# Kernel tuning notes

Measured on AMD Instinct MI355X. Metric: run time of the kernel, lower is better.

## Reference

```python
import jax, jax.numpy as jnp
import numpy as np

NUM_GRAPHS = 512  # number of segments (graphs) in the batch
NEG_SLOPE = 0.01  # nn.LeakyReLU default


def setup_inputs() -> dict:
    key = jax.random.key(0)
    k1, k2, k3, k4, k5 = jax.random.split(key, 5)
    N, D = 200000, 128
    h_topo = jax.random.normal(k1, (N, D), dtype=jnp.float32)
    h_geom = jax.random.normal(k2, (N, D), dtype=jnp.float32)
    batch = jnp.sort(jax.random.randint(k3, (N,), 0, NUM_GRAPHS, dtype=jnp.int64))
    concat_dim, hidden, out_dim = 6 * D, 2 * D, 128
    W1 = jax.random.normal(k4, (concat_dim, hidden), dtype=jnp.float32) * 0.02
    b1 = jnp.zeros((hidden,), dtype=jnp.float32)
    W2 = jax.random.normal(k5, (hidden, out_dim), dtype=jnp.float32) * 0.02
    b2 = jnp.zeros((out_dim,), dtype=jnp.float32)
    return {"h_topo": h_topo, "h_geom": h_geom, "batch": batch,
            "W1": W1, "b1": b1, "W2": W2, "b2": b2}


def _pool_feats(h, batch):
    # global_max_pool / global_mean_pool keyed by graph id, gathered back per node
    gmax = jax.ops.segment_max(h, batch, num_segments=NUM_GRAPHS)
    gsum = jax.ops.segment_sum(h, batch, num_segments=NUM_GRAPHS)
    cnt = jax.ops.segment_sum(jnp.ones((h.shape[0],), h.dtype), batch,
                              num_segments=NUM_GRAPHS)
    gmean = gsum / jnp.maximum(cnt, 1.0)[:, None]
    return gmax[batch], gmean[batch]  # [N, D] each


def reference(h_topo, h_geom, batch, W1, b1, W2, b2):
    t_max, t_mean = _pool_feats(h_topo, batch)
    g_max, g_mean = _pool_feats(h_geom, batch)
    # [Topo, Geom, TopoMax, TopoMean, GeomMax, GeomMean]
    combined = jnp.concatenate(
        [h_topo, t_max, t_mean, h_geom, g_max, g_mean], axis=-1)  # [N, 6D]
    h = combined @ W1 + b1
    h = jnp.where(h >= 0, h, NEG_SLOPE * h)  # LeakyReLU
    return h @ W2 + b2
```

## Files before the change

### kernel.cpp

```cpp
#include <hip/hip_runtime.h>
#include <math.h>

#define NUM_GRAPHS 512
#define D 128
#define NEG 0.01f
#define BN 128
#define NS 4

typedef __attribute__((ext_vector_type(8))) short  bf16x8;
typedef __attribute__((ext_vector_type(4))) float  f32x4;
typedef __attribute__((ext_vector_type(4))) int    i32x4;

__device__ __forceinline__ unsigned short f2bf(float f) {
    unsigned u = __float_as_uint(f);
    u += 0x7fffu + ((u >> 16) & 1u);
    return (unsigned short)(u >> 16);
}

__device__ __forceinline__ bf16x8 cvt8(float4 a, float4 b) {
    unsigned w0, w1, w2, w3;
    asm("v_cvt_pk_bf16_f32 %0, %1, %2" : "=v"(w0) : "v"(a.x), "v"(a.y));
    asm("v_cvt_pk_bf16_f32 %0, %1, %2" : "=v"(w1) : "v"(a.z), "v"(a.w));
    asm("v_cvt_pk_bf16_f32 %0, %1, %2" : "=v"(w2) : "v"(b.x), "v"(b.y));
    asm("v_cvt_pk_bf16_f32 %0, %1, %2" : "=v"(w3) : "v"(b.z), "v"(b.w));
    i32x4 v; v[0] = (int)w0; v[1] = (int)w1; v[2] = (int)w2; v[3] = (int)w3;
    return __builtin_bit_cast(bf16x8, v);
}

__device__ __forceinline__ int swz128(int row, int k) {
    return (row >> 6) * 16384 + (row & 63) * 256 + (k ^ ((row & 7) << 3));
}

#define LDS_BARRIER()                                                        \
    do {                                                                     \
        asm volatile("s_waitcnt lgkmcnt(0)" ::: "memory");                   \
        __builtin_amdgcn_s_barrier();                                        \
        asm volatile("" ::: "memory");                                       \
    } while (0)

#define FMAX4(a, b)                                                          \
    do {                                                                     \
        (a).x = fmaxf((a).x, (b).x); (a).y = fmaxf((a).y, (b).y);            \
        (a).z = fmaxf((a).z, (b).z); (a).w = fmaxf((a).w, (b).w);            \
    } while (0)
#define FADD4(a, b)                                                          \
    do {                                                                     \
        (a).x += (b).x; (a).y += (b).y; (a).z += (b).z; (a).w += (b).w;      \
    } while (0)

__global__ __launch_bounds__(256) void bounds_kernel(
    const int* __restrict__ batch, int N, int* __restrict__ seg)
{
    const int g = blockIdx.x * 256 + threadIdx.x;
    if (g <= NUM_GRAPHS) {
        int lo = 0, hi = N;
        while (lo < hi) { int m = (lo + hi) >> 1; if (batch[m] < g) lo = m + 1; else hi = m; }
        seg[g] = lo;
    }
}

__global__ __launch_bounds__(256) void pool_kernel(
    const float* __restrict__ h_topo, const float* __restrict__ h_geom,
    const int* __restrict__ seg, int N, float* __restrict__ pp)
{
    const int g = blockIdx.x, t = blockIdx.y, s = blockIdx.z;
    const float* __restrict__ h = t ? h_geom : h_topo;

    const int start = seg[g], end = seg[g + 1];
    const int len = end - start;
    const int r0  = start + (int)(((long long)len * s) / NS);
    const int r1  = start + (int)(((long long)len * (s + 1)) / NS);

    const int c = threadIdx.x & 31;
    const int r = threadIdx.x >> 5;

    float4 mxA = make_float4(-INFINITY, -INFINITY, -INFINITY, -INFINITY);
    float4 mxB = mxA, mxC = mxA, mxD = mxA;
    float4 smA = make_float4(0.f, 0.f, 0.f, 0.f);
    float4 smB = smA, smC = smA, smD = smA;

    int row = r0 + r;
    for (; row + 24 < r1; row += 32) {
        float4 v0 = *(const float4*)(h + (size_t)row * D + c * 4);
        float4 v1 = *(const float4*)(h + (size_t)(row + 8)  * D + c * 4);
        float4 v2 = *(const float4*)(h + (size_t)(row + 16) * D + c * 4);
        float4 v3 = *(const float4*)(h + (size_t)(row + 24) * D + c * 4);
        FMAX4(mxA, v0); FADD4(smA, v0);
        FMAX4(mxB, v1); FADD4(smB, v1);
        FMAX4(mxC, v2); FADD4(smC, v2);
        FMAX4(mxD, v3); FADD4(smD, v3);
    }
    for (; row < r1; row += 8) {
        float4 v = *(const float4*)(h + (size_t)row * D + c * 4);
        FMAX4(mxA, v); FADD4(smA, v);
    }
    FMAX4(mxA, mxB); FMAX4(mxC, mxD); FMAX4(mxA, mxC);
    FADD4(smA, smB); FADD4(smC, smD); FADD4(smA, smC);

    __shared__ float4 smx[256], ssm[256];
    smx[threadIdx.x] = mxA; ssm[threadIdx.x] = smA;
    __syncthreads();
    #pragma unroll
    for (int st = 4; st > 0; st >>= 1) {
        if (r < st) {
            float4 a = smx[threadIdx.x + st * 32];
            float4 b = ssm[threadIdx.x + st * 32];
            float4 m0 = smx[threadIdx.x];
            float4 s0 = ssm[threadIdx.x];
            FMAX4(m0, a); FADD4(s0, b);
            smx[threadIdx.x] = m0; ssm[threadIdx.x] = s0;
        }
        __syncthreads();
    }
    if (r == 0) {
        float* dst = pp + ((size_t)(g * 2 + t) * NS + s) * 256;
        *(float4*)(dst + c * 4)       = smx[threadIdx.x];
        *(float4*)(dst + 128 + c * 4) = ssm[threadIdx.x];
    }
}

__global__ __launch_bounds__(256) void pmat_kernel(
    const float* __restrict__ pp, const int* __restrict__ seg,
    const float* __restrict__ W1, const float* __restrict__ b1,
    float* __restrict__ P)
{
    const int g = blockIdx.x;
    const int j = threadIdx.x;

    const int start = seg[g], end = seg[g + 1];
    const float inv   = 1.0f / fmaxf((float)(end - start), 1.0f);
    const bool  empty = (end <= start);

    __shared__ float pl[512];
    #pragma unroll
    for (int e0 = 0; e0 < 2; ++e0) {
        const int e = j + e0 * 256;
        const int t = e >> 8, i = e & 255;
        const float* q = pp + (size_t)(g * 2 + t) * NS * 256 + i;
        float v;
        if (i < 128)
            v = fmaxf(fmaxf(q[0], q[256]), fmaxf(q[512], q[768]));
        else
            v = (q[0] + q[256] + q[512] + q[768]) * inv;
        pl[e] = empty ? 0.f : v;
    }
    __syncthreads();

    float acc = b1[j];
    #pragma unroll 8
    for (int k = 0; k < 256; ++k)
        acc += pl[k] * W1[(size_t)(128 + k) * 256 + j];
    #pragma unroll 8
    for (int k = 0; k < 256; ++k)
        acc += pl[256 + k] * W1[(size_t)(512 + k) * 256 + j];

    P[(size_t)g * 256 + j] = acc;
}

__global__ __launch_bounds__(256) void wconv_kernel(
    const float* __restrict__ W1, const float* __restrict__ W2,
    unsigned short* __restrict__ W1bT, unsigned short* __restrict__ W2bT)
{
    const int idx = blockIdx.x * 256 + threadIdx.x;
    if (idx < 256 * 256) {
        const int n = idx >> 8, k = idx & 255;
        const int kk = (k < 128) ? k : (k + 256);
        W1bT[idx] = f2bf(W1[(size_t)kk * 256 + n]);
    } else {
        const int j = idx - 256 * 256;
        if (j < 128 * 256) {
            const int n = j >> 8, k = j & 255;
            W2bT[j] = f2bf(W2[(size_t)k * 128 + n]);
        }
    }
}

__global__ __launch_bounds__(512, 4) void mlp_mfma(
    const float* __restrict__ h_topo, const float* __restrict__ h_geom,
    const int* __restrict__ batch, const float* __restrict__ P,
    const unsigned short* __restrict__ W1bT, const unsigned short* __restrict__ W2bT,
    const float* __restrict__ b2, float* __restrict__ out, int N)
{
    __shared__ unsigned short xs[128 * 256];
    __shared__ int gid[128];

    const int tid  = threadIdx.x;
    const int wave = tid >> 6, lane = tid & 63;
    const int base = (gridDim.x - 1 - blockIdx.x) * BN;

    {
        const int row  = tid >> 2, kq = tid & 3;
        const int node = min(base + row, N - 1);
        const float* src = (kq < 2) ? h_topo + (size_t)node * D + kq * 64
                                    : h_geom + (size_t)node * D + (kq - 2) * 64;
        #pragma unroll
        for (int i = 0; i < 8; ++i) {
            float4 a = ((const float4*)src)[2 * i];
            float4 b = ((const float4*)src)[2 * i + 1];
            *(bf16x8*)&xs[swz128(row, kq * 64 + i * 8)] = cvt8(a, b);
        }
    }
    if (tid < 128) gid[tid] = batch[min(base + tid, N - 1)];

    const int g0 = batch[base];
    const int g1 = batch[min(base + 127, N - 1)];
    const bool uni = (g0 == g1);

    const int lhi = lane >> 4;
    const int llo = lane & 15;

    const int wr = wave >> 2, wc = wave & 3;

    const unsigned short* w1p = W1bT + (size_t)(wc * 64 + llo) * 256 + lhi * 8;

    float4 pf4[4];
    if (uni) {
        #pragma unroll
        for (int ct = 0; ct < 4; ++ct)
            pf4[ct] = *(const float4*)(P + (size_t)g0 * 256 + wc * 64 + ct * 16 + lhi * 4);
    }

    bf16x8 aW[2][4];
    #pragma unroll
    for (int ct = 0; ct < 4; ++ct) {
        aW[0][ct] = *(const bf16x8*)(w1p + (size_t)ct * 16 * 256);
        aW[1][ct] = *(const bf16x8*)(w1p + (size_t)ct * 16 * 256 + 32);
    }

    LDS_BARRIER();

    f32x4 acc[4][4];
    #pragma unroll
    for (int rt = 0; rt < 4; ++rt)
        #pragma unroll
        for (int ct = 0; ct < 4; ++ct)
            acc[rt][ct] = uni ? (f32x4){pf4[ct].x, pf4[ct].y, pf4[ct].z, pf4[ct].w}
                              : (f32x4){0.f, 0.f, 0.f, 0.f};

    #pragma unroll
    for (int ks = 0; ks < 8; ++ks) {
        const int kb = ks * 32 + lhi * 8;
        bf16x8 bX[4];
        #pragma unroll
        for (int rt = 0; rt < 4; ++rt)
            bX[rt] = *(const bf16x8*)&xs[swz128(wr * 64 + rt * 16 + llo, kb)];
        __builtin_amdgcn_s_setprio(1);
        #pragma unroll
        for (int rt = 0; rt < 4; ++rt)
            #pragma unroll
            for (int ct = 0; ct < 4; ++ct)
                acc[rt][ct] = __builtin_amdgcn_mfma_f32_16x16x32_bf16(
                    aW[ks & 1][ct], bX[rt], acc[rt][ct], 0, 0, 0);
        __builtin_amdgcn_s_setprio(0);
        if (ks < 6) {
            const int kbn = (ks + 2) * 32;
            #pragma unroll
            for (int ct = 0; ct < 4; ++ct)
                aW[ks & 1][ct] = *(const bf16x8*)(w1p + (size_t)ct * 16 * 256 + kbn);
        }
    }

    const int wr2 = wave >> 2, wc2 = wave & 3;
    const unsigned short* w2pA = W2bT + (size_t)(wc2 * 32 + llo) * 256 + lhi * 8;
    const unsigned short* w2pB = W2bT + (size_t)(wc2 * 32 + 16 + llo) * 256 + lhi * 8;

    bf16x8 aW2[2][2];
    aW2[0][0] = *(const bf16x8*)(w2pA);
    aW2[0][1] = *(const bf16x8*)(w2pB);
    aW2[1][0] = *(const bf16x8*)(w2pA + 32);
    aW2[1][1] = *(const bf16x8*)(w2pB + 32);

    LDS_BARRIER();

    #pragma unroll
    for (int rt = 0; rt < 4; ++rt) {
        const int nrow = wr * 64 + rt * 16 + llo;
        int gg = 0;
        if (!uni) gg = gid[nrow];
        #pragma unroll
        for (int ct = 0; ct < 4; ++ct) {
            const int j0 = wc * 64 + ct * 16 + lhi * 4;
            float4 v = make_float4(acc[rt][ct][0], acc[rt][ct][1],
                                   acc[rt][ct][2], acc[rt][ct][3]);
            if (!uni) {
                float4 pv = *(const float4*)(P + (size_t)gg * 256 + j0);
                v.x += pv.x; v.y += pv.y; v.z += pv.z; v.w += pv.w;
            }
            v.x = fmaxf(v.x, NEG * v.x); v.y = fmaxf(v.y, NEG * v.y);
            v.z = fmaxf(v.z, NEG * v.z); v.w = fmaxf(v.w, NEG * v.w);
            unsigned w0, w1;
            asm("v_cvt_pk_bf16_f32 %0, %1, %2" : "=v"(w0) : "v"(v.x), "v"(v.y));
            asm("v_cvt_pk_bf16_f32 %0, %1, %2" : "=v"(w1) : "v"(v.z), "v"(v.w));
            uint2 hw; hw.x = w0; hw.y = w1;
            *(uint2*)&xs[swz128(nrow, j0)] = hw;
        }
    }

    LDS_BARRIER();

    f32x4 acc2[4][2];
    {
        const float4 bbA = *(const float4*)(b2 + wc2 * 32 + lhi * 4);
        const float4 bbB = *(const float4*)(b2 + wc2 * 32 + 16 + lhi * 4);
        #pragma unroll
        for (int nt = 0; nt < 4; ++nt) {
            acc2[nt][0] = (f32x4){bbA.x, bbA.y, bbA.z, bbA.w};
            acc2[nt][1] = (f32x4){bbB.x, bbB.y, bbB.z, bbB.w};
        }
    }
    #pragma unroll
    for (int ks = 0; ks < 8; ++ks) {
        const int kb = ks * 32 + lhi * 8;
        bf16x8 bH[4];
        #pragma unroll
        for (int nt = 0; nt < 4; ++nt)
            bH[nt] = *(const bf16x8*)&xs[swz128(wr2 * 64 + nt * 16 + llo, kb)];
        __builtin_amdgcn_s_setprio(1);
        #pragma unroll
        for (int nt = 0; nt < 4; ++nt) {
            acc2[nt][0] = __builtin_amdgcn_mfma_f32_16x16x32_bf16(
                aW2[ks & 1][0], bH[nt], acc2[nt][0], 0, 0, 0);
            acc2[nt][1] = __builtin_amdgcn_mfma_f32_16x16x32_bf16(
                aW2[ks & 1][1], bH[nt], acc2[nt][1], 0, 0, 0);
        }
        __builtin_amdgcn_s_setprio(0);
        if (ks < 6) {
            aW2[ks & 1][0] = *(const bf16x8*)(w2pA + (ks + 2) * 32);
            aW2[ks & 1][1] = *(const bf16x8*)(w2pB + (ks + 2) * 32);
        }
    }

    #pragma unroll
    for (int nt = 0; nt < 4; ++nt) {
        const int node = base + wr2 * 64 + nt * 16 + llo;
        if (node < N) {
            float* op = out + (size_t)node * 128 + wc2 * 32 + lhi * 4;
            __builtin_nontemporal_store(acc2[nt][0], (f32x4*)op);
            __builtin_nontemporal_store(acc2[nt][1], (f32x4*)(op + 16));
        }
    }
}

extern "C" void kernel_launch(void* const* d_in, const int* in_sizes, int n_in,
                              void* d_out, int out_size, void* d_ws, size_t ws_size,
                              hipStream_t stream)
{
    const float* h_topo = (const float*)d_in[0];
    const float* h_geom = (const float*)d_in[1];
    const int*   batch  = (const int*)  d_in[2];
    const float* W1     = (const float*)d_in[3];
    const float* b1     = (const float*)d_in[4];
    const float* W2     = (const float*)d_in[5];
    const float* b2     = (const float*)d_in[6];
    float* out = (float*)d_out;

    const int N = in_sizes[0] / D;

    float*          pp   = (float*)d_ws;
    float*          P    = pp + (size_t)NUM_GRAPHS * 2 * NS * 256;
    unsigned short* W1bT = (unsigned short*)(P + (size_t)NUM_GRAPHS * 256);
    unsigned short* W2bT = W1bT + 256 * 256;
    int*            seg  = (int*)(W2bT + 128 * 256);

    bounds_kernel<<<3, 256, 0, stream>>>(batch, N, seg);
    wconv_kernel<<<(256 * 256 + 128 * 256) / 256, 256, 0, stream>>>(W1, W2, W1bT, W2bT);
    pool_kernel<<<dim3(NUM_GRAPHS, 2, NS), 256, 0, stream>>>(h_topo, h_geom, seg, N, pp);
    pmat_kernel<<<NUM_GRAPHS, 256, 0, stream>>>(pp, seg, W1, b1, P);

    const int nblocks = (N + BN - 1) / BN;
    mlp_mfma<<<nblocks, 512, 0, stream>>>(h_topo, h_geom, batch, P,
                                          W1bT, W2bT, b2, out, N);
}
```

Before: 194.0 us.

## Halve MLP row tile, swap MFMA operand roles, and split pooling eightfold

The fused MLP kernel now processes 64 nodes per 256-thread block instead of 128 nodes per 512-thread block. Each wave owns a 64-column slice of the hidden layer across all 64 rows, and the MFMA operand order is swapped so node rows come from LDS as the A operand. The hidden-activation epilogue now adds the per-graph term, applies LeakyReLU and writes bf16 to LDS one element at a time instead of packed pairs. The pooling split factor rises from 4 to 8, and the reduce kernel loops over the partials. The aim is more blocks in flight with less LDS per block, at the cost of loading the weight tiles twice as often per node and narrower LDS stores.

```diff
diff --git a/kernel.cpp b/kernel.cpp
--- a/kernel.cpp
+++ b/kernel.cpp
@@ -4,8 +4,8 @@
 #define NUM_GRAPHS 512
 #define D 128
 #define NEG 0.01f
-#define BN 128
-#define NS 4
+#define BN 64
+#define NS 8
 
 typedef __attribute__((ext_vector_type(8))) short  bf16x8;
 typedef __attribute__((ext_vector_type(4))) float  f32x4;
@@ -27,8 +27,8 @@
     return __builtin_bit_cast(bf16x8, v);
 }
 
-__device__ __forceinline__ int swz128(int row, int k) {
-    return (row >> 6) * 16384 + (row & 63) * 256 + (k ^ ((row & 7) << 3));
+__device__ __forceinline__ int swz64(int row, int k) {
+    return row * 256 + (k ^ ((row & 7) << 3));
 }
 
 #define LDS_BARRIER()                                                        \
@@ -138,10 +138,16 @@
         const int t = e >> 8, i = e & 255;
         const float* q = pp + (size_t)(g * 2 + t) * NS * 256 + i;
         float v;
-        if (i < 128)
-            v = fmaxf(fmaxf(q[0], q[256]), fmaxf(q[512], q[768]));
-        else
-            v = (q[0] + q[256] + q[512] + q[768]) * inv;
+        if (i < 128) {
+            v = q[0];
+            #pragma unroll
+            for (int s = 1; s < NS; ++s) v = fmaxf(v, q[s * 256]);
+        } else {
+            v = q[0];
+            #pragma unroll
+            for (int s = 1; s < NS; ++s) v += q[s * 256];
+            v *= inv;
+        }
         pl[e] = empty ? 0.f : v;
     }
     __syncthreads();
@@ -175,14 +181,14 @@
     }
 }
 
-__global__ __launch_bounds__(512, 4) void mlp_mfma(
+__global__ __launch_bounds__(256, 4) void mlp_mfma(
     const float* __restrict__ h_topo, const float* __restrict__ h_geom,
     const int* __restrict__ batch, const float* __restrict__ P,
     const unsigned short* __restrict__ W1bT, const unsigned short* __restrict__ W2bT,
     const float* __restrict__ b2, float* __restrict__ out, int N)
 {
-    __shared__ unsigned short xs[128 * 256];
-    __shared__ int gid[128];
+    __shared__ unsigned short xs[64 * 256];
+    __shared__ int gid[64];
 
     const int tid  = threadIdx.x;
     const int wave = tid >> 6, lane = tid & 63;
@@ -197,34 +203,32 @@
         for (int i = 0; i < 8; ++i) {
             float4 a = ((const float4*)src)[2 * i];
             float4 b = ((const float4*)src)[2 * i + 1];
-            *(bf16x8*)&xs[swz128(row, kq * 64 + i * 8)] = cvt8(a, b);
-        }
-    }
-    if (tid < 128) gid[tid] = batch[min(base + tid, N - 1)];
+            *(bf16x8*)&xs[swz64(row, kq * 64 + i * 8)] = cvt8(a, b);
+        }
+    }
+    if (tid < 64) gid[tid] = batch[min(base + tid, N - 1)];
 
     const int g0 = batch[base];
-    const int g1 = batch[min(base + 127, N - 1)];
+    const int g1 = batch[min(base + 63, N - 1)];
     const bool uni = (g0 == g1);
 
     const int lhi = lane >> 4;
     const int llo = lane & 15;
 
-    const int wr = wave >> 2, wc = wave & 3;
-
-    const unsigned short* w1p = W1bT + (size_t)(wc * 64 + llo) * 256 + lhi * 8;
-
-    float4 pf4[4];
+    const unsigned short* w1p = W1bT + (size_t)(wave * 64 + llo) * 256 + lhi * 8;
+
+    float pf[4];
     if (uni) {
         #pragma unroll
         for (int ct = 0; ct < 4; ++ct)
-            pf4[ct] = *(const float4*)(P + (size_t)g0 * 256 + wc * 64 + ct * 16 + lhi * 4);
-    }
-
-    bf16x8 aW[2][4];
+            pf[ct] = P[(size_t)g0 * 256 + wave * 64 + ct * 16 + llo];
+    }
+
+    bf16x8 bfr[2][4];
     #pragma unroll
     for (int ct = 0; ct < 4; ++ct) {
-        aW[0][ct] = *(const bf16x8*)(w1p + (size_t)ct * 16 * 256);
-        aW[1][ct] = *(const bf16x8*)(w1p + (size_t)ct * 16 * 256 + 32);
+        bfr[0][ct] = *(const bf16x8*)(w1p + (size_t)ct * 16 * 256);
+        bfr[1][ct] = *(const bf16x8*)(w1p + (size_t)ct * 16 * 256 + 32);
     }
 
     LDS_BARRIER();
@@ -233,36 +237,36 @@
     #pragma unroll
     for (int rt = 0; rt < 4; ++rt)
         #pragma unroll
-        for (int ct = 0; ct < 4; ++ct)
-            acc[rt][ct] = uni ? (f32x4){pf4[ct].x, pf4[ct].y, pf4[ct].z, pf4[ct].w}
-                              : (f32x4){0.f, 0.f, 0.f, 0.f};
+        for (int ct = 0; ct < 4; ++ct) {
+            const float p = uni ? pf[ct] : 0.f;
+            acc[rt][ct] = (f32x4){p, p, p, p};
+        }
 
     #pragma unroll
     for (int ks = 0; ks < 8; ++ks) {
         const int kb = ks * 32 + lhi * 8;
-        bf16x8 bX[4];
+        bf16x8 afr[4];
         #pragma unroll
         for (int rt = 0; rt < 4; ++rt)
-            bX[rt] = *(const bf16x8*)&xs[swz128(wr * 64 + rt * 16 + llo, kb)];
+            afr[rt] = *(const bf16x8*)&xs[swz64(rt * 16 + llo, kb)];
         __builtin_amdgcn_s_setprio(1);
         #pragma unroll
         for (int rt = 0; rt < 4; ++rt)
             #pragma unroll
             for (int ct = 0; ct < 4; ++ct)
                 acc[rt][ct] = __builtin_amdgcn_mfma_f32_16x16x32_bf16(
-                    aW[ks & 1][ct], bX[rt], acc[rt][ct], 0, 0, 0);
+                    afr[rt], bfr[ks & 1][ct], acc[rt][ct], 0, 0, 0);
         __builtin_amdgcn_s_setprio(0);
         if (ks < 6) {
             const int kbn = (ks + 2) * 32;
             #pragma unroll
             for (int ct = 0; ct < 4; ++ct)
-                aW[ks & 1][ct] = *(const bf16x8*)(w1p + (size_t)ct * 16 * 256 + kbn);
-        }
-    }
-
-    const int wr2 = wave >> 2, wc2 = wave & 3;
-    const unsigned short* w2pA = W2bT + (size_t)(wc2 * 32 + llo) * 256 + lhi * 8;
-    const unsigned short* w2pB = W2bT + (size_t)(wc2 * 32 + 16 + llo) * 256 + lhi * 8;
+                bfr[ks & 1][ct] = *(const bf16x8*)(w1p + (size_t)ct * 16 * 256 + kbn);
+        }
+    }
+
+    const unsigned short* w2pA = W2bT + (size_t)(wave * 32 + llo) * 256 + lhi * 8;
+    const unsigned short* w2pB = W2bT + (size_t)(wave * 32 + 16 + llo) * 256 + lhi * 8;
 
     bf16x8 aW2[2][2];
     aW2[0][0] = *(const bf16x8*)(w2pA);
@@ -274,25 +278,17 @@
 
     #pragma unroll
     for (int rt = 0; rt < 4; ++rt) {
-        const int nrow = wr * 64 + rt * 16 + llo;
-        int gg = 0;
-        if (!uni) gg = gid[nrow];
         #pragma unroll
         for (int ct = 0; ct < 4; ++ct) {
-            const int j0 = wc * 64 + ct * 16 + lhi * 4;
-            float4 v = make_float4(acc[rt][ct][0], acc[rt][ct][1],
-                                   acc[rt][ct][2], acc[rt][ct][3]);
-            if (!uni) {
-                float4 pv = *(const float4*)(P + (size_t)gg * 256 + j0);
-                v.x += pv.x; v.y += pv.y; v.z += pv.z; v.w += pv.w;
+            const int col = wave * 64 + ct * 16 + llo;
+            #pragma unroll
+            for (int q = 0; q < 4; ++q) {
+                const int row = rt * 16 + lhi * 4 + q;
+                float v = acc[rt][ct][q];
+                if (!uni) v += P[(size_t)gid[row] * 256 + col];
+                v = fmaxf(v, NEG * v);
+                xs[swz64(row, col)] = f2bf(v);
             }
-            v.x = fmaxf(v.x, NEG * v.x); v.y = fmaxf(v.y, NEG * v.y);
-            v.z = fmaxf(v.z, NEG * v.z); v.w = fmaxf(v.w, NEG * v.w);
-            unsigned w0, w1;
-            asm("v_cvt_pk_bf16_f32 %0, %1, %2" : "=v"(w0) : "v"(v.x), "v"(v.y));
-            asm("v_cvt_pk_bf16_f32 %0, %1, %2" : "=v"(w1) : "v"(v.z), "v"(v.w));
-            uint2 hw; hw.x = w0; hw.y = w1;
-            *(uint2*)&xs[swz128(nrow, j0)] = hw;
         }
     }
 
@@ -300,8 +296,8 @@
 
     f32x4 acc2[4][2];
     {
-        const float4 bbA = *(const float4*)(b2 + wc2 * 32 + lhi * 4);
-        const float4 bbB = *(const float4*)(b2 + wc2 * 32 + 16 + lhi * 4);
+        const float4 bbA = *(const float4*)(b2 + wave * 32 + lhi * 4);
+        const float4 bbB = *(const float4*)(b2 + wave * 32 + 16 + lhi * 4);
         #pragma unroll
         for (int nt = 0; nt < 4; ++nt) {
             acc2[nt][0] = (f32x4){bbA.x, bbA.y, bbA.z, bbA.w};
@@ -314,7 +310,7 @@
         bf16x8 bH[4];
         #pragma unroll
         for (int nt = 0; nt < 4; ++nt)
-            bH[nt] = *(const bf16x8*)&xs[swz128(wr2 * 64 + nt * 16 + llo, kb)];
+            bH[nt] = *(const bf16x8*)&xs[swz64(nt * 16 + llo, kb)];
         __builtin_amdgcn_s_setprio(1);
         #pragma unroll
         for (int nt = 0; nt < 4; ++nt) {
@@ -332,9 +328,9 @@
 
     #pragma unroll
     for (int nt = 0; nt < 4; ++nt) {
-        const int node = base + wr2 * 64 + nt * 16 + llo;
+        const int node = base + nt * 16 + llo;
         if (node < N) {
-            float* op = out + (size_t)node * 128 + wc2 * 32 + lhi * 4;
+            float* op = out + (size_t)node * 128 + wave * 32 + lhi * 4;
             __builtin_nontemporal_store(acc2[nt][0], (f32x4*)op);
             __builtin_nontemporal_store(acc2[nt][1], (f32x4*)(op + 16));
         }
@@ -368,6 +364,6 @@
     pmat_kernel<<<NUM_GRAPHS, 256, 0, stream>>>(pp, seg, W1, b1, P);
 
     const int nblocks = (N + BN - 1) / BN;
-    mlp_mfma<<<nblocks, 512, 0, stream>>>(h_topo, h_geom, batch, P,
+    mlp_mfma<<<nblocks, 256, 0, stream>>>(h_topo, h_geom, batch, P,
                                           W1bT, W2bT, b2, out, N);
 }
```

Measured after the change: 187.0 us. -3.6%, faster.
